# Optimization experiments

Measured on AMD Instinct MI355X. Metric: run time of the kernel, lower is better.

Reference implementation:

```python
import jax, jax.numpy as jnp
import numpy as np

K = 1024
H = 16

def setup_inputs() -> dict:
    key = jax.random.key(0)
    ks = jax.random.split(key, 6)
    s = 1.0 / np.sqrt(K)
    return {
        "x": jax.random.normal(ks[0], (2, 2048, K), dtype=jnp.float32),
        "Wq": jax.random.uniform(ks[1], (K, K), jnp.float32, -s, s),
        "Wk": jax.random.uniform(ks[2], (K, K), jnp.float32, -s, s),
        "Wv": jax.random.uniform(ks[3], (K, K), jnp.float32, -s, s),
        "Wu": jax.random.uniform(ks[4], (K, K), jnp.float32, -s, s),
        "bu": jax.random.uniform(ks[5], (K,), jnp.float32, -s, s),
    }

def reference(x, Wq, Wk, Wv, Wu, bu):
    b, t, k = x.shape
    hd = k // H  # head dim = 64
    scale = jnp.asarray(k, x.dtype) ** 0.25  # Bloem-style: scale q and k each by k^(1/4)
    # nn.Linear(bias=False): y = x @ W.T
    q = (jnp.einsum('btk,ok->bto', x, Wq) / scale).reshape(b, t, H, hd)
    kk = (jnp.einsum('btk,ok->bto', x, Wk) / scale).reshape(b, t, H, hd)
    v = jnp.einsum('btk,ok->bto', x, Wv).reshape(b, t, H, hd)
    dot = jnp.einsum('bthd,bshd->bhts', q, kk)  # [b,h,t,t]
    att = jax.nn.softmax(dot, axis=-1)
    out = jnp.einsum('bhts,bshd->bthd', att, v).reshape(b, t, k)
    return jnp.einsum('btk,ok->bto', out, Wu) + bu
```

## Files before the change

### kernel.cpp

```cpp
#include <hip/hip_runtime.h>

typedef __bf16 bf16;
typedef bf16  bf16x8 __attribute__((ext_vector_type(8)));
typedef bf16  bf16x4 __attribute__((ext_vector_type(4)));
typedef float f32x4  __attribute__((ext_vector_type(4)));

#define MFMA16(a, b, c) __builtin_amdgcn_mfma_f32_16x16x32_bf16((a), (b), (c), 0, 0, 0)
#define AS1 __attribute__((address_space(1)))
#define AS3 __attribute__((address_space(3)))

__device__ __forceinline__ void gld_lds16(const bf16* g, bf16* l) {
    __builtin_amdgcn_global_load_lds((AS1 void*)(g), (AS3 void*)(l), 16, 0, 0);
}


__global__ __launch_bounds__(256) void cvt_all(const float* __restrict__ x,
                                               const float* __restrict__ Wq, const float* __restrict__ Wk,
                                               const float* __restrict__ Wv, const float* __restrict__ Wu,
                                               bf16* ox, bf16* oq, bf16* ok, bf16* ov, bf16* ou,
                                               float sq, float sk) {
    int bid = blockIdx.x;
    const float* src; bf16* dst; float sc; int base;
    if (bid < 4096) { src = x; dst = ox; sc = 1.0f; base = bid; }
    else {
        int w = (bid - 4096) >> 10; base = (bid - 4096) & 1023;
        switch (w) {
            case 0:  src = Wq; dst = oq; sc = sq;   break;
            case 1:  src = Wk; dst = ok; sc = sk;   break;
            case 2:  src = Wv; dst = ov; sc = 1.0f; break;
            default: src = Wu; dst = ou; sc = 1.0f; break;
        }
    }
    int idx = (base * 256 + threadIdx.x) * 4;
    float4 v = *(const float4*)(src + idx);
    bf16x4 o;
    o[0] = (bf16)(v.x * sc); o[1] = (bf16)(v.y * sc);
    o[2] = (bf16)(v.z * sc); o[3] = (bf16)(v.w * sc);
    *(bf16x4*)(dst + idx) = o;
}

__device__ __forceinline__ void gemm_core(const bf16* __restrict__ A, const bf16* __restrict__ B,
                                          int mBase, int nBase,
                                          bf16 (*As)[128][32], bf16 (*Bs)[128][32],
                                          f32x4 acc[4][4]) {
    const int tid = threadIdx.x;
    const int wave = tid >> 6, lane = tid & 63;
    const int g = lane >> 4, lr = lane & 15;
    const int wm = (wave & 1) << 6, wn = (wave >> 1) << 6;
    const int q = lane >> 2;
    const int cswz = ((lane & 3) ^ ((lane >> 3) & 3)) << 3;
    const int pcs  = (g ^ ((lr >> 1) & 3)) << 3;

    const int bi0 = wave << 2;

    for (int k0 = 0; k0 < 1024; k0 += 64) {
        __syncthreads();
#pragma unroll
        for (int i = 0; i < 4; i++) {
            int bi = bi0 + i;
            int p = bi >> 3, rb = (bi & 7) << 4;
            int kof = k0 + (p << 5) + cswz;
            gld_lds16(A + (size_t)(mBase + rb + q) * 1024 + kof, &As[p][rb][0]);
            gld_lds16(B + (size_t)(nBase + rb + q) * 1024 + kof, &Bs[p][rb][0]);
        }
        __syncthreads();

#pragma unroll
        for (int ks = 0; ks < 2; ks++) {
            bf16x8 af[4], bfr[4];
#pragma unroll
            for (int i = 0; i < 4; i++)
                af[i] = *(const bf16x8*)&As[ks][wm + (i << 4) + lr][pcs];
#pragma unroll
            for (int j = 0; j < 4; j++)
                bfr[j] = *(const bf16x8*)&Bs[ks][wn + (j << 4) + lr][pcs];
#pragma unroll
            for (int i = 0; i < 4; i++)
#pragma unroll
                for (int j = 0; j < 4; j++)
                    acc[i][j] = MFMA16(af[i], bfr[j], acc[i][j]);
        }
    }
}

__global__ __launch_bounds__(256) void gemm_qkv(const bf16* __restrict__ A,
                                                const bf16* __restrict__ Wq, const bf16* __restrict__ Wk,
                                                const bf16* __restrict__ Wv,
                                                bf16* __restrict__ Qo, bf16* __restrict__ Ko,
                                                bf16* __restrict__ Vto) {
    __shared__ bf16 As[2][128][32];
    __shared__ bf16 Bs[2][128][32];
    const int tid = threadIdx.x;
    const int wave = tid >> 6, lane = tid & 63;
    const int g = lane >> 4, lr = lane & 15;
    const int wm = (wave & 1) << 6, wn = (wave >> 1) << 6;
    const int z = blockIdx.z;

    const bf16 *Ap, *Bp;
    int mBase, nBase;
    if (z == 2) { Ap = Wv; Bp = A;            mBase = blockIdx.x * 128; nBase = blockIdx.y * 128; }
    else        { Ap = A;  Bp = z ? Wk : Wq;  mBase = blockIdx.y * 128; nBase = blockIdx.x * 128; }

    f32x4 acc[4][4] = {};
    gemm_core(Ap, Bp, mBase, nBase, As, Bs, acc);

#pragma unroll
    for (int i = 0; i < 4; i++)
#pragma unroll
        for (int j = 0; j < 4; j++)
#pragma unroll
            for (int r = 0; r < 4; r++) {
                int m = mBase + wm + (i << 4) + (g << 2) + r;
                int n = nBase + wn + (j << 4) + lr;
                bf16 v = (bf16)acc[i][j][r];
                if (z == 2) {
                    int h = m >> 6, d = m & 63, b = n >> 11, t = n & 2047;
                    Vto[((size_t)(((b << 4) + h) << 6) + d) * 2048 + t] = v;
                } else {
                    int b = m >> 11, t = m & 2047, h = n >> 6, d = n & 63;
                    bf16* dst = (z == 0) ? Qo : Ko;
                    dst[(((size_t)((b << 4) + h) * 2048 + t) << 6) + d] = v;
                }
            }
}

__global__ __launch_bounds__(256) void gemm_out(const bf16* __restrict__ A, const bf16* __restrict__ B,
                                                const float* __restrict__ bias, float* __restrict__ out) {
    __shared__ bf16 As[2][128][32];
    __shared__ bf16 Bs[2][128][32];
    const int tid = threadIdx.x;
    const int wave = tid >> 6, lane = tid & 63;
    const int g = lane >> 4, lr = lane & 15;
    const int wm = (wave & 1) << 6, wn = (wave >> 1) << 6;
    const int mBase = blockIdx.y * 128, nBase = blockIdx.x * 128;

    f32x4 acc[4][4] = {};
    gemm_core(A, B, mBase, nBase, As, Bs, acc);

#pragma unroll
    for (int i = 0; i < 4; i++)
#pragma unroll
        for (int j = 0; j < 4; j++) {
            int n = nBase + wn + (j << 4) + lr;
            float bv = bias[n];
#pragma unroll
            for (int r = 0; r < 4; r++) {
                int m = mBase + wm + (i << 4) + (g << 2) + r;
                out[((size_t)m << 10) + n] = acc[i][j][r] + bv;
            }
        }
}

__global__ __launch_bounds__(256) void attn(const bf16* __restrict__ Q, const bf16* __restrict__ Kt,
                                            const bf16* __restrict__ Vt, bf16* __restrict__ O) {
    __shared__ bf16 Qs[2][128][32];
    __shared__ bf16 Ks[2][128][32];
    __shared__ bf16 Vs[4][64][32];
    bf16 (*Ps)[32][32] = (bf16(*)[32][32]) & Qs[0][0][0];

    const int tid = threadIdx.x;
    const int wave = tid >> 6, lane = tid & 63;
    const int g = lane >> 4, lr = lane & 15;
    const int q = lane >> 2;
    const int cswz = ((lane & 3) ^ ((lane >> 3) & 3)) << 3;
    const int pcs  = (g ^ ((lr >> 1) & 3)) << 3;
    const int pw0 = ((((g >> 1))     ^ ((lr >> 1) & 3)) << 3) + ((g & 1) << 2);
    const int pw1 = (((2 + (g >> 1)) ^ ((lr >> 1) & 3)) << 3) + ((g & 1) << 2);

    const int bh = blockIdx.y;
    const int qBase = blockIdx.x << 7;

    const bf16* Qg = Q + ((size_t)bh * 2048 + qBase) * 64;
    const bf16* Kg = Kt + (size_t)bh * 2048 * 64;
    const bf16* Vg = Vt + (size_t)bh * 64 * 2048;

#pragma unroll
    for (int i = 0; i < 4; i++) {
        int bi = (wave << 2) + i;
        int p = bi >> 3, rb = (bi & 7) << 4;
        gld_lds16(Qg + (rb + q) * 64 + (p << 5) + cswz, &Qs[p][rb][0]);
    }
    __syncthreads();

    bf16x8 qf[2][2];
#pragma unroll
    for (int ks = 0; ks < 2; ks++)
#pragma unroll
        for (int tt = 0; tt < 2; tt++)
            qf[ks][tt] = *(const bf16x8*)&Qs[ks][(wave << 5) + (tt << 4) + lr][pcs];

    bf16x8 ones;
#pragma unroll
    for (int i = 0; i < 8; i++) ones[i] = (bf16)1.0f;

    f32x4 oacc[2][4] = {};
    f32x4 oaccL[2] = {};

    for (int s0 = 0; s0 < 2048; s0 += 128) {
        __syncthreads();
#pragma unroll
        for (int i = 0; i < 4; i++) {
            int bi = (wave << 2) + i;
            {
                int p = bi >> 3, rb = (bi & 7) << 4;
                gld_lds16(Kg + (size_t)(s0 + rb + q) * 64 + (p << 5) + cswz, &Ks[p][rb][0]);
            }
            {
                int p = bi >> 2, rb = (bi & 3) << 4;
                gld_lds16(Vg + (size_t)(rb + q) * 2048 + s0 + (p << 5) + cswz, &Vs[p][rb][0]);
            }
        }
        __syncthreads();

#pragma unroll
        for (int ks2 = 0; ks2 < 4; ks2++) {
            f32x4 sacc[2][2] = {};
#pragma unroll
            for (int isub = 0; isub < 2; isub++) {
                int is = (ks2 << 1) + isub;
#pragma unroll
                for (int ks = 0; ks < 2; ks++) {
                    bf16x8 kf = *(const bf16x8*)&Ks[ks][(is << 4) + lr][pcs];
                    sacc[isub][0] = MFMA16(kf, qf[ks][0], sacc[isub][0]);
                    sacc[isub][1] = MFMA16(kf, qf[ks][1], sacc[isub][1]);
                }
            }
#pragma unroll
            for (int isub = 0; isub < 2; isub++)
#pragma unroll
                for (int tt = 0; tt < 2; tt++) {
                    f32x4 s = sacc[isub][tt];
                    bf16x4 pb;
                    pb[0] = (bf16)__builtin_amdgcn_exp2f(s[0]);
                    pb[1] = (bf16)__builtin_amdgcn_exp2f(s[1]);
                    pb[2] = (bf16)__builtin_amdgcn_exp2f(s[2]);
                    pb[3] = (bf16)__builtin_amdgcn_exp2f(s[3]);
                    *(bf16x4*)&Ps[wave][(tt << 4) + lr][isub ? pw1 : pw0] = pb;
                }
            bf16x8 pf0 = *(const bf16x8*)&Ps[wave][lr][pcs];
            bf16x8 pf1 = *(const bf16x8*)&Ps[wave][16 + lr][pcs];
#pragma unroll
            for (int jd = 0; jd < 4; jd++) {
                bf16x8 vf = *(const bf16x8*)&Vs[ks2][(jd << 4) + lr][pcs];
                oacc[0][jd] = MFMA16(pf0, vf, oacc[0][jd]);
                oacc[1][jd] = MFMA16(pf1, vf, oacc[1][jd]);
            }
            oaccL[0] = MFMA16(pf0, ones, oaccL[0]);
            oaccL[1] = MFMA16(pf1, ones, oaccL[1]);
        }
    }

    float linv[2][4];
#pragma unroll
    for (int tt = 0; tt < 2; tt++)
#pragma unroll
        for (int r = 0; r < 4; r++)
            linv[tt][r] = 1.0f / oaccL[tt][r];

    const int b = bh >> 4, h = bh & 15;
#pragma unroll
    for (int tt = 0; tt < 2; tt++)
#pragma unroll
        for (int jd = 0; jd < 4; jd++)
#pragma unroll
            for (int r = 0; r < 4; r++) {
                int t = qBase + (wave << 5) + (tt << 4) + (g << 2) + r;
                int col = (h << 6) + (jd << 4) + lr;
                O[(((size_t)(b * 2048 + t)) << 10) + col] = (bf16)(oacc[tt][jd][r] * linv[tt][r]);
            }
}

extern "C" void kernel_launch(void* const* d_in, const int* in_sizes, int n_in,
                              void* d_out, int out_size, void* d_ws, size_t ws_size,
                              hipStream_t stream) {
    const float* x  = (const float*)d_in[0];
    const float* Wq = (const float*)d_in[1];
    const float* Wk = (const float*)d_in[2];
    const float* Wv = (const float*)d_in[3];
    const float* Wu = (const float*)d_in[4];
    const float* bu = (const float*)d_in[5];
    float* out = (float*)d_out;

    char* ws = (char*)d_ws;
    bf16* xbf  = (bf16*)(ws);
    bf16* wqbf = (bf16*)(ws + ((size_t)8  << 20));
    bf16* wkbf = (bf16*)(ws + ((size_t)10 << 20));
    bf16* wvbf = (bf16*)(ws + ((size_t)12 << 20));
    bf16* wubf = (bf16*)(ws + ((size_t)14 << 20));
    bf16* Qb   = (bf16*)(ws + ((size_t)16 << 20));
    bf16* Kb   = (bf16*)(ws + ((size_t)24 << 20));
    bf16* Vtb  = (bf16*)(ws + ((size_t)32 << 20));
    bf16* attnO = xbf;

    const float iscale_k = 0.17677669529663687f;
    const float iscale_q = 0.25503540109f;

    cvt_all<<<8192, 256, 0, stream>>>(x, Wq, Wk, Wv, Wu, xbf, wqbf, wkbf, wvbf, wubf,
                                      iscale_q, iscale_k);

    gemm_qkv<<<dim3(8, 32, 3), 256, 0, stream>>>(xbf, wqbf, wkbf, wvbf, Qb, Kb, Vtb);
    attn<<<dim3(16, 32), 256, 0, stream>>>(Qb, Kb, Vtb, attnO);
    gemm_out<<<dim3(8, 32), 256, 0, stream>>>(attnO, wubf, bu, out);
}
```

Before: 205.7 us.

## Halve attention query tile, remap grid for locality, shrink GEMM K-step

```diff
diff --git a/kernel.cpp b/kernel.cpp
--- a/kernel.cpp
+++ b/kernel.cpp
@@ -40,8 +40,7 @@
 }
 
 __device__ __forceinline__ void gemm_core(const bf16* __restrict__ A, const bf16* __restrict__ B,
-                                          int mBase, int nBase,
-                                          bf16 (*As)[128][32], bf16 (*Bs)[128][32],
+                                          int mBase, int nBase, bf16* As, bf16* Bs,
                                           f32x4 acc[4][4]) {
     const int tid = threadIdx.x;
     const int wave = tid >> 6, lane = tid & 63;
@@ -51,35 +50,32 @@
     const int cswz = ((lane & 3) ^ ((lane >> 3) & 3)) << 3;
     const int pcs  = (g ^ ((lr >> 1) & 3)) << 3;
 
-    const int bi0 = wave << 2;
-
-    for (int k0 = 0; k0 < 1024; k0 += 64) {
-        __syncthreads();
-#pragma unroll
-        for (int i = 0; i < 4; i++) {
-            int bi = bi0 + i;
-            int p = bi >> 3, rb = (bi & 7) << 4;
-            int kof = k0 + (p << 5) + cswz;
-            gld_lds16(A + (size_t)(mBase + rb + q) * 1024 + kof, &As[p][rb][0]);
-            gld_lds16(B + (size_t)(nBase + rb + q) * 1024 + kof, &Bs[p][rb][0]);
-        }
-        __syncthreads();
-
-#pragma unroll
-        for (int ks = 0; ks < 2; ks++) {
-            bf16x8 af[4], bfr[4];
-#pragma unroll
-            for (int i = 0; i < 4; i++)
-                af[i] = *(const bf16x8*)&As[ks][wm + (i << 4) + lr][pcs];
+    const int rb0 = wave << 4, rb1 = rb0 + 64;
+    const bf16* a0 = A + (size_t)(mBase + rb0 + q) * 1024 + cswz;
+    const bf16* a1 = A + (size_t)(mBase + rb1 + q) * 1024 + cswz;
+    const bf16* b0 = B + (size_t)(nBase + rb0 + q) * 1024 + cswz;
+    const bf16* b1 = B + (size_t)(nBase + rb1 + q) * 1024 + cswz;
+
+    for (int k0 = 0; k0 < 1024; k0 += 32) {
+        __syncthreads();
+        gld_lds16(a0 + k0, As + rb0 * 32);
+        gld_lds16(a1 + k0, As + rb1 * 32);
+        gld_lds16(b0 + k0, Bs + rb0 * 32);
+        gld_lds16(b1 + k0, Bs + rb1 * 32);
+        __syncthreads();
+
+        bf16x8 af[4], bfr[4];
+#pragma unroll
+        for (int i = 0; i < 4; i++)
+            af[i] = *(const bf16x8*)&As[(wm + (i << 4) + lr) * 32 + pcs];
+#pragma unroll
+        for (int j = 0; j < 4; j++)
+            bfr[j] = *(const bf16x8*)&Bs[(wn + (j << 4) + lr) * 32 + pcs];
+#pragma unroll
+        for (int i = 0; i < 4; i++)
 #pragma unroll
             for (int j = 0; j < 4; j++)
-                bfr[j] = *(const bf16x8*)&Bs[ks][wn + (j << 4) + lr][pcs];
-#pragma unroll
-            for (int i = 0; i < 4; i++)
-#pragma unroll
-                for (int j = 0; j < 4; j++)
-                    acc[i][j] = MFMA16(af[i], bfr[j], acc[i][j]);
-        }
+                acc[i][j] = MFMA16(af[i], bfr[j], acc[i][j]);
     }
 }
 
@@ -88,8 +84,8 @@
                                                 const bf16* __restrict__ Wv,
                                                 bf16* __restrict__ Qo, bf16* __restrict__ Ko,
                                                 bf16* __restrict__ Vto) {
-    __shared__ bf16 As[2][128][32];
-    __shared__ bf16 Bs[2][128][32];
+    __shared__ bf16 As[128 * 32];
+    __shared__ bf16 Bs[128 * 32];
     const int tid = threadIdx.x;
     const int wave = tid >> 6, lane = tid & 63;
     const int g = lane >> 4, lr = lane & 15;
@@ -126,8 +122,8 @@
 
 __global__ __launch_bounds__(256) void gemm_out(const bf16* __restrict__ A, const bf16* __restrict__ B,
                                                 const float* __restrict__ bias, float* __restrict__ out) {
-    __shared__ bf16 As[2][128][32];
-    __shared__ bf16 Bs[2][128][32];
+    __shared__ bf16 As[128 * 32];
+    __shared__ bf16 Bs[128 * 32];
     const int tid = threadIdx.x;
     const int wave = tid >> 6, lane = tid & 63;
     const int g = lane >> 4, lr = lane & 15;
@@ -151,12 +147,12 @@
         }
 }
 
-__global__ __launch_bounds__(256) void attn(const bf16* __restrict__ Q, const bf16* __restrict__ Kt,
-                                            const bf16* __restrict__ Vt, bf16* __restrict__ O) {
-    __shared__ bf16 Qs[2][128][32];
+__global__ __launch_bounds__(256, 4) void attn(const bf16* __restrict__ Q, const bf16* __restrict__ Kt,
+                                               const bf16* __restrict__ Vt, bf16* __restrict__ O) {
+    __shared__ bf16 Qs[2][64][32];
     __shared__ bf16 Ks[2][128][32];
     __shared__ bf16 Vs[4][64][32];
-    bf16 (*Ps)[32][32] = (bf16(*)[32][32]) & Qs[0][0][0];
+    bf16 (*Ps)[16][32] = (bf16(*)[16][32]) & Qs[0][0][0];
 
     const int tid = threadIdx.x;
     const int wave = tid >> 6, lane = tid & 63;
@@ -167,34 +163,34 @@
     const int pw0 = ((((g >> 1))     ^ ((lr >> 1) & 3)) << 3) + ((g & 1) << 2);
     const int pw1 = (((2 + (g >> 1)) ^ ((lr >> 1) & 3)) << 3) + ((g & 1) << 2);
 
-    const int bh = blockIdx.y;
-    const int qBase = blockIdx.x << 7;
+    const int bid = blockIdx.x;
+    const int bh = ((bid & 7) << 2) | (bid >> 8);
+    const int qt = (bid >> 3) & 31;
+    const int qBase = qt << 6;
 
     const bf16* Qg = Q + ((size_t)bh * 2048 + qBase) * 64;
     const bf16* Kg = Kt + (size_t)bh * 2048 * 64;
     const bf16* Vg = Vt + (size_t)bh * 64 * 2048;
 
 #pragma unroll
-    for (int i = 0; i < 4; i++) {
-        int bi = (wave << 2) + i;
-        int p = bi >> 3, rb = (bi & 7) << 4;
+    for (int i = 0; i < 2; i++) {
+        int bi = (wave << 1) + i;
+        int p = bi >> 2, rb = (bi & 3) << 4;
         gld_lds16(Qg + (rb + q) * 64 + (p << 5) + cswz, &Qs[p][rb][0]);
     }
     __syncthreads();
 
-    bf16x8 qf[2][2];
+    bf16x8 qf[2];
 #pragma unroll
     for (int ks = 0; ks < 2; ks++)
-#pragma unroll
-        for (int tt = 0; tt < 2; tt++)
-            qf[ks][tt] = *(const bf16x8*)&Qs[ks][(wave << 5) + (tt << 4) + lr][pcs];
+        qf[ks] = *(const bf16x8*)&Qs[ks][(wave << 4) + lr][pcs];
 
     bf16x8 ones;
 #pragma unroll
     for (int i = 0; i < 8; i++) ones[i] = (bf16)1.0f;
 
-    f32x4 oacc[2][4] = {};
-    f32x4 oaccL[2] = {};
+    f32x4 oacc[4] = {};
+    f32x4 oaccL = {};
 
     for (int s0 = 0; s0 < 2048; s0 += 128) {
         __syncthreads();
@@ -214,60 +210,49 @@
 
 #pragma unroll
         for (int ks2 = 0; ks2 < 4; ks2++) {
-            f32x4 sacc[2][2] = {};
+            f32x4 sacc[2] = {};
 #pragma unroll
             for (int isub = 0; isub < 2; isub++) {
                 int is = (ks2 << 1) + isub;
 #pragma unroll
                 for (int ks = 0; ks < 2; ks++) {
                     bf16x8 kf = *(const bf16x8*)&Ks[ks][(is << 4) + lr][pcs];
-                    sacc[isub][0] = MFMA16(kf, qf[ks][0], sacc[isub][0]);
-                    sacc[isub][1] = MFMA16(kf, qf[ks][1], sacc[isub][1]);
+                    sacc[isub] = MFMA16(kf, qf[ks], sacc[isub]);
                 }
             }
 #pragma unroll
-            for (int isub = 0; isub < 2; isub++)
-#pragma unroll
-                for (int tt = 0; tt < 2; tt++) {
-                    f32x4 s = sacc[isub][tt];
-                    bf16x4 pb;
-                    pb[0] = (bf16)__builtin_amdgcn_exp2f(s[0]);
-                    pb[1] = (bf16)__builtin_amdgcn_exp2f(s[1]);
-                    pb[2] = (bf16)__builtin_amdgcn_exp2f(s[2]);
-                    pb[3] = (bf16)__builtin_amdgcn_exp2f(s[3]);
-                    *(bf16x4*)&Ps[wave][(tt << 4) + lr][isub ? pw1 : pw0] = pb;
-                }
-            bf16x8 pf0 = *(const bf16x8*)&Ps[wave][lr][pcs];
-            bf16x8 pf1 = *(const bf16x8*)&Ps[wave][16 + lr][pcs];
+            for (int isub = 0; isub < 2; isub++) {
+                f32x4 s = sacc[isub];
+                bf16x4 pb;
+                pb[0] = (bf16)__builtin_amdgcn_exp2f(s[0]);
+                pb[1] = (bf16)__builtin_amdgcn_exp2f(s[1]);
+                pb[2] = (bf16)__builtin_amdgcn_exp2f(s[2]);
+                pb[3] = (bf16)__builtin_amdgcn_exp2f(s[3]);
+                *(bf16x4*)&Ps[wave][lr][isub ? pw1 : pw0] = pb;
+            }
+            bf16x8 pf = *(const bf16x8*)&Ps[wave][lr][pcs];
 #pragma unroll
             for (int jd = 0; jd < 4; jd++) {
                 bf16x8 vf = *(const bf16x8*)&Vs[ks2][(jd << 4) + lr][pcs];
-                oacc[0][jd] = MFMA16(pf0, vf, oacc[0][jd]);
-                oacc[1][jd] = MFMA16(pf1, vf, oacc[1][jd]);
-            }
-            oaccL[0] = MFMA16(pf0, ones, oaccL[0]);
-            oaccL[1] = MFMA16(pf1, ones, oaccL[1]);
-        }
-    }
-
-    float linv[2][4];
-#pragma unroll
-    for (int tt = 0; tt < 2; tt++)
-#pragma unroll
-        for (int r = 0; r < 4; r++)
-            linv[tt][r] = 1.0f / oaccL[tt][r];
+                oacc[jd] = MFMA16(pf, vf, oacc[jd]);
+            }
+            oaccL = MFMA16(pf, ones, oaccL);
+        }
+    }
+
+    float linv[4];
+#pragma unroll
+    for (int r = 0; r < 4; r++) linv[r] = 1.0f / oaccL[r];
 
     const int b = bh >> 4, h = bh & 15;
 #pragma unroll
-    for (int tt = 0; tt < 2; tt++)
-#pragma unroll
-        for (int jd = 0; jd < 4; jd++)
-#pragma unroll
-            for (int r = 0; r < 4; r++) {
-                int t = qBase + (wave << 5) + (tt << 4) + (g << 2) + r;
-                int col = (h << 6) + (jd << 4) + lr;
-                O[(((size_t)(b * 2048 + t)) << 10) + col] = (bf16)(oacc[tt][jd][r] * linv[tt][r]);
-            }
+    for (int jd = 0; jd < 4; jd++)
+#pragma unroll
+        for (int r = 0; r < 4; r++) {
+            int t = qBase + (wave << 4) + (g << 2) + r;
+            int col = (h << 6) + (jd << 4) + lr;
+            O[(((size_t)(b * 2048 + t)) << 10) + col] = (bf16)(oacc[jd][r] * linv[r]);
+        }
 }
 
 extern "C" void kernel_launch(void* const* d_in, const int* in_sizes, int n_in,
@@ -299,6 +284,6 @@
                                       iscale_q, iscale_k);
 
     gemm_qkv<<<dim3(8, 32, 3), 256, 0, stream>>>(xbf, wqbf, wkbf, wvbf, Qb, Kb, Vtb);
-    attn<<<dim3(16, 32), 256, 0, stream>>>(Qb, Kb, Vtb, attnO);
+    attn<<<dim3(1024), 256, 0, stream>>>(Qb, Kb, Vtb, attnO);
     gemm_out<<<dim3(8, 32), 256, 0, stream>>>(attnO, wubf, bu, out);
 }
```

New measurement: 193.8 us. 5.8% less time.
